# Optimization experiments

Measured on AMD Instinct MI355X. Metric: run time of the kernel, lower is better.

The kernel has to match this reference:

```python
import jax, jax.numpy as jnp
import numpy as np

D_MODEL, D_K, D_V = 1024, 64, 64
B, S = 4, 4096

def setup_inputs() -> dict:
    key = jax.random.key(0)
    ks = jax.random.split(key, 9)
    s_in = 1.0 / np.sqrt(D_MODEL)
    return {
        "Q": jax.random.normal(ks[0], (B, S, D_MODEL), jnp.float32),
        "K": jax.random.normal(ks[1], (B, S, D_MODEL), jnp.float32),
        "V": jax.random.normal(ks[2], (B, S, D_MODEL), jnp.float32),
        "Wq": jax.random.uniform(ks[3], (D_MODEL, D_K), jnp.float32, -s_in, s_in),
        "bq": jax.random.uniform(ks[4], (D_K,), jnp.float32, -s_in, s_in),
        "Wk": jax.random.uniform(ks[5], (D_MODEL, D_K), jnp.float32, -s_in, s_in),
        "bk": jax.random.uniform(ks[6], (D_K,), jnp.float32, -s_in, s_in),
        "Wv": jax.random.uniform(ks[7], (D_MODEL, D_V), jnp.float32, -s_in, s_in),
        "bv": jax.random.uniform(ks[8], (D_V,), jnp.float32, -s_in, s_in),
    }

def reference(Q, K, V, Wq, bq, Wk, bk, Wv, bv):
    # Linear projections: [B,S,d_model] -> [B,S,d_k/d_v]
    q = jnp.einsum("bsm,mk->bsk", Q, Wq) + bq
    k = jnp.einsum("btm,mk->btk", K, Wk) + bk
    v = jnp.einsum("btm,mv->btv", V, Wv) + bv
    # Scaled dot-product attention, softmax over key axis (dim=2)
    scores = jnp.einsum("bsk,btk->bst", q, k) / jnp.sqrt(jnp.float32(D_K))
    attn = jax.nn.softmax(scores, axis=2)  # [B,S,S]
    return jnp.einsum("bst,btv->bsv", attn, v)
```

## Files before the change

### kernel.cpp

```cpp
#include <hip/hip_runtime.h>

typedef __bf16 bf16;
typedef __attribute__((ext_vector_type(8))) __bf16 bf16x8;
typedef __attribute__((ext_vector_type(4))) float f32x4;
typedef __attribute__((ext_vector_type(16))) float f32x16;

#define MFMA16(a, b, c) __builtin_amdgcn_mfma_f32_16x16x32_bf16((a), (b), (c), 0, 0, 0)
#define MFMA32(a, b, c) __builtin_amdgcn_mfma_f32_32x32x16_bf16((a), (b), (c), 0, 0, 0)

__device__ __forceinline__ bf16 tobf(float f) {
    unsigned u = __float_as_uint(f);
    u += 0x7fffu + ((u >> 16) & 1u);
    unsigned short h = (unsigned short)(u >> 16);
    bf16 r;
    __builtin_memcpy(&r, &h, 2);
    return r;
}

__device__ __forceinline__ bf16x8 cvt8h(f32x4 a, f32x4 b) {
    bf16x8 r;
    r[0] = (bf16)a[0]; r[1] = (bf16)a[1]; r[2] = (bf16)a[2]; r[3] = (bf16)a[3];
    r[4] = (bf16)b[0]; r[5] = (bf16)b[1]; r[6] = (bf16)b[2]; r[7] = (bf16)b[3];
    return r;
}

__global__ void wconv_kernel(const float* __restrict__ Wq, const float* __restrict__ Wk,
                             const float* __restrict__ Wv, bf16* __restrict__ Wt) {
    int j = blockIdx.y;
    const float* W = (j == 0) ? Wq : ((j == 1) ? Wk : Wv);
    int idx = blockIdx.x * 256 + threadIdx.x;
    int m = idx >> 6, n = idx & 63;
    Wt[(size_t)j * 65536 + (size_t)n * 1024 + m] = tobf(W[idx]);
}

__launch_bounds__(256, 4)
__global__ void proj_kernel(const float* __restrict__ Q, const float* __restrict__ K,
                            const float* __restrict__ V, const bf16* __restrict__ Wt,
                            const float* __restrict__ bq, const float* __restrict__ bk,
                            const float* __restrict__ bv,
                            bf16* __restrict__ q_ws, bf16* __restrict__ k_ws,
                            bf16* __restrict__ vT_ws) {
    const int j = blockIdx.y;
    const float* In   = (j == 0) ? Q : ((j == 1) ? K : V);
    const float* bias = (j == 0) ? bq : ((j == 1) ? bk : bv);
    const bf16* W = Wt + (size_t)j * 65536;

    __shared__ bf16 vtile[64][72];

    const int tid = threadIdx.x;
    const int wave = tid >> 6, lane = tid & 63;
    const int quad = lane >> 4, l16 = lane & 15;
    const int rbase = blockIdx.x * 64 + wave * 16;

    const float* arow = In + (size_t)(rbase + l16) * 1024 + quad * 8;
    const bf16* wbase = W + quad * 8;

    f32x4 acc[4];
#pragma unroll
    for (int nt = 0; nt < 4; nt++) acc[nt] = {0.f, 0.f, 0.f, 0.f};

    f32x4 a0 = *(const f32x4*)(arow);
    f32x4 a1 = *(const f32x4*)(arow + 4);
    f32x4 a2 = *(const f32x4*)(arow + 32);
    f32x4 a3 = *(const f32x4*)(arow + 36);

    for (int kc = 0; kc < 1024; kc += 64) {
        bf16x8 av0 = cvt8h(a0, a1);
        bf16x8 av1 = cvt8h(a2, a3);
        if (kc + 64 < 1024) {
            a0 = *(const f32x4*)(arow + kc + 64);
            a1 = *(const f32x4*)(arow + kc + 68);
            a2 = *(const f32x4*)(arow + kc + 96);
            a3 = *(const f32x4*)(arow + kc + 100);
        }
#pragma unroll
        for (int nt = 0; nt < 4; nt++) {
            const bf16* wp = wbase + (size_t)(nt * 16 + l16) * 1024 + kc;
            bf16x8 b0 = *(const bf16x8*)(wp);
            bf16x8 b1 = *(const bf16x8*)(wp + 32);
            acc[nt] = MFMA16(av0, b0, acc[nt]);
            acc[nt] = MFMA16(av1, b1, acc[nt]);
        }
    }

    const float scale = (j == 0) ? 0.125f * 1.44269504088896f : 1.0f;

    if (j != 2) {
        bf16* dst = (j == 0) ? q_ws : k_ws;
#pragma unroll
        for (int nt = 0; nt < 4; nt++) {
            int n = nt * 16 + l16;
            float bb = bias[n];
#pragma unroll
            for (int r = 0; r < 4; r++) {
                int row = rbase + quad * 4 + r;
                dst[(size_t)row * 64 + n] = tobf((acc[nt][r] + bb) * scale);
            }
        }
    } else {
#pragma unroll
        for (int nt = 0; nt < 4; nt++) {
            int n = nt * 16 + l16;
            float bb = bias[n];
#pragma unroll
            for (int r = 0; r < 4; r++) {
                vtile[n][wave * 16 + quad * 4 + r] = tobf(acc[nt][r] + bb);
            }
        }
        __syncthreads();
        int gb = blockIdx.x * 64;
        int bi = gb >> 12, t0 = gb & 4095;
        int d = tid >> 2, part = (tid & 3) * 16;
        bf16x8 x0 = *(const bf16x8*)&vtile[d][part];
        bf16x8 x1 = *(const bf16x8*)&vtile[d][part + 8];
        bf16* dst = vT_ws + (size_t)(bi * 64 + d) * 4096 + t0 + part;
        *(bf16x8*)dst = x0;
        *(bf16x8*)(dst + 8) = x1;
    }
}

__launch_bounds__(256, 3)
__global__ void attn_kernel(const bf16* __restrict__ q_ws, const bf16* __restrict__ k_ws,
                            const bf16* __restrict__ vT_ws,
                            float* __restrict__ po, float* __restrict__ pl,
                            float* __restrict__ out, int keys_per_split, int direct) {
    const int b = blockIdx.z, split = blockIdx.y;
    const int tid = threadIdx.x, wave = tid >> 6, lane = tid & 63;
    const int l32 = lane & 31, h = lane >> 5;

    __shared__ bf16 kt[64][80];
    __shared__ bf16 vt[64][80];
    __shared__ bf16 pt[4][32][72];

    const int qrow0 = b * 4096 + blockIdx.x * 128 + wave * 32;

    bf16x8 qf[4];
    const bf16* qp = q_ws + (size_t)(qrow0 + l32) * 64 + h * 8;
#pragma unroll
    for (int c = 0; c < 4; c++) qf[c] = *(const bf16x8*)(qp + c * 16);

    f32x16 o0, o1;
    float l[16];
#pragma unroll
    for (int i = 0; i < 16; i++) { o0[i] = 0.f; o1[i] = 0.f; l[i] = 0.f; }

    const int key0 = split * keys_per_split;
    const int srow = tid >> 3, scol = (tid & 7) * 8;
    const bf16* kg = k_ws + (size_t)(b * 4096 + key0 + srow) * 64 + scol;
    const bf16* vg = vT_ws + (size_t)(b * 64 + srow) * 4096 + key0 + scol;

    uint4 kv0 = *(const uint4*)kg;
    uint4 kv1 = *(const uint4*)(kg + 2048);
    uint4 vv0 = *(const uint4*)vg;
    uint4 vv1 = *(const uint4*)(vg + 131072);

    for (int t0 = 0; t0 < keys_per_split; t0 += 64) {
        __syncthreads();
        *(uint4*)&kt[srow][scol]      = kv0;
        *(uint4*)&kt[srow + 32][scol] = kv1;
        *(uint4*)&vt[srow][scol]      = vv0;
        *(uint4*)&vt[srow + 32][scol] = vv1;
        if (t0 + 64 < keys_per_split) {
            kv0 = *(const uint4*)(kg + (size_t)(t0 + 64) * 64);
            kv1 = *(const uint4*)(kg + (size_t)(t0 + 64) * 64 + 2048);
            vv0 = *(const uint4*)(vg + t0 + 64);
            vv1 = *(const uint4*)(vg + t0 + 64 + 131072);
        }
        __syncthreads();

#pragma unroll
        for (int kt32 = 0; kt32 < 2; kt32++) {
            f32x16 s;
#pragma unroll
            for (int i = 0; i < 16; i++) s[i] = 0.f;
#pragma unroll
            for (int c = 0; c < 4; c++) {
                bf16x8 kf = *(const bf16x8*)(&kt[kt32 * 32 + l32][c * 16 + h * 8]);
                s = MFMA32(qf[c], kf, s);
            }
#pragma unroll
            for (int i = 0; i < 16; i++) {
                float p = __builtin_amdgcn_exp2f(s[i]);
                l[i] += p;
                int R = (i & 3) + 8 * (i >> 2) + 4 * h;
                pt[wave][R][kt32 * 32 + l32] = (bf16)p;
            }
        }

#pragma unroll
        for (int tc = 0; tc < 4; tc++) {
            bf16x8 pf  = *(const bf16x8*)(&pt[wave][l32][tc * 16 + h * 8]);
            bf16x8 vf0 = *(const bf16x8*)(&vt[l32][tc * 16 + h * 8]);
            bf16x8 vf1 = *(const bf16x8*)(&vt[32 + l32][tc * 16 + h * 8]);
            o0 = MFMA32(pf, vf0, o0);
            o1 = MFMA32(pf, vf1, o1);
        }
    }

#pragma unroll
    for (int i = 0; i < 16; i++) {
        float v = l[i];
        v += __shfl_xor(v, 1);  v += __shfl_xor(v, 2);  v += __shfl_xor(v, 4);
        v += __shfl_xor(v, 8);  v += __shfl_xor(v, 16);
        l[i] = v;
    }

    if (direct) {
        float* orow = out + (size_t)qrow0 * 64;
#pragma unroll
        for (int i = 0; i < 16; i++) {
            int R = (i & 3) + 8 * (i >> 2) + 4 * h;
            float inv = 1.0f / l[i];
            orow[(size_t)R * 64 + l32]      = o0[i] * inv;
            orow[(size_t)R * 64 + 32 + l32] = o1[i] * inv;
        }
    } else {
        size_t prow = (size_t)split * 16384 + qrow0;
        float* pob = po + prow * 64;
#pragma unroll
        for (int i = 0; i < 16; i++) {
            int R = (i & 3) + 8 * (i >> 2) + 4 * h;
            pob[(size_t)R * 64 + l32]      = o0[i];
            pob[(size_t)R * 64 + 32 + l32] = o1[i];
            if (l32 == 0) pl[prow + R] = l[i];
        }
    }
}

__launch_bounds__(256)
__global__ void combine_kernel(const float* __restrict__ po, const float* __restrict__ pl,
                               float* __restrict__ out, int nsplit) {
    int idx = blockIdx.x * 256 + threadIdx.x;
    int row = idx >> 6;
    float so = 0.f, sl = 0.f;
    for (int s = 0; s < nsplit; s++) {
        so += po[(size_t)s * 1048576 + idx];
        sl += pl[(size_t)s * 16384 + row];
    }
    out[idx] = so / sl;
}

extern "C" void kernel_launch(void* const* d_in, const int* in_sizes, int n_in,
                              void* d_out, int out_size, void* d_ws, size_t ws_size,
                              hipStream_t stream) {
    const float* Q  = (const float*)d_in[0];
    const float* K  = (const float*)d_in[1];
    const float* V  = (const float*)d_in[2];
    const float* Wq = (const float*)d_in[3];
    const float* bq = (const float*)d_in[4];
    const float* Wk = (const float*)d_in[5];
    const float* bk = (const float*)d_in[6];
    const float* Wv = (const float*)d_in[7];
    const float* bv = (const float*)d_in[8];
    float* out = (float*)d_out;

    char* ws = (char*)d_ws;
    bf16* Wt    = (bf16*)ws;
    bf16* q_ws  = (bf16*)(ws + 393216);
    bf16* k_ws  = (bf16*)(ws + 393216 + 2097152);
    bf16* vT_ws = (bf16*)(ws + 393216 + 2 * 2097152);
    const size_t base = 393216 + 3 * 2097152;

    const size_t per_split = 16384u * 4u + 1048576u * 4u;
    int nsplit = 1;
    if (ws_size >= base + 8 * per_split) nsplit = 8;
    else if (ws_size >= base + 4 * per_split) nsplit = 4;
    else if (ws_size >= base + 2 * per_split) nsplit = 2;

    float* pl = (float*)(ws + base);
    float* po = (float*)(ws + base + (size_t)nsplit * 65536);

    hipLaunchKernelGGL(wconv_kernel, dim3(256, 3), dim3(256), 0, stream, Wq, Wk, Wv, Wt);
    hipLaunchKernelGGL(proj_kernel, dim3(256, 3), dim3(256), 0, stream,
                       Q, K, V, Wt, bq, bk, bv, q_ws, k_ws, vT_ws);
    hipLaunchKernelGGL(attn_kernel, dim3(32, nsplit, 4), dim3(256), 0, stream,
                       q_ws, k_ws, vT_ws, po, pl, out, 4096 / nsplit, nsplit == 1 ? 1 : 0);
    if (nsplit > 1) {
        hipLaunchKernelGGL(combine_kernel, dim3(4096), dim3(256), 0, stream, po, pl, out, nsplit);
    }
}
```

Baseline: 273.7 us.

## Stage projection tiles through LDS with direct global-to-LDS loads and XOR swizzle

The projection kernel now copies 64x128 fp32 input tiles and 64x128 bf16 weight tiles into shared memory using global_load_lds with an XOR swizzle, then feeds the MFMAs from LDS. Before, each lane read global memory directly with a register prefetch. The aim is coalesced bulk loads and weight reuse across the four waves, at the cost of two barriers per k-chunk and no overlap between loading and compute. Launch bounds are also swapped (proj to 3 blocks per CU, attn to 4), and attn's K/V LDS row padding shrinks from 80 to 72.

```diff
diff --git a/kernel.cpp b/kernel.cpp
--- a/kernel.cpp
+++ b/kernel.cpp
@@ -7,6 +7,13 @@
 
 #define MFMA16(a, b, c) __builtin_amdgcn_mfma_f32_16x16x32_bf16((a), (b), (c), 0, 0, 0)
 #define MFMA32(a, b, c) __builtin_amdgcn_mfma_f32_32x32x16_bf16((a), (b), (c), 0, 0, 0)
+
+typedef __attribute__((address_space(3))) unsigned int lds_u32_t;
+typedef __attribute__((address_space(1))) unsigned int glb_u32_t;
+
+__device__ __forceinline__ void gl2lds16(const void* g, void* l) {
+    __builtin_amdgcn_global_load_lds((const glb_u32_t*)g, (lds_u32_t*)l, 16, 0, 0);
+}
 
 __device__ __forceinline__ bf16 tobf(float f) {
     unsigned u = __float_as_uint(f);
@@ -33,7 +40,7 @@
     Wt[(size_t)j * 65536 + (size_t)n * 1024 + m] = tobf(W[idx]);
 }
 
-__launch_bounds__(256, 4)
+__launch_bounds__(256, 3)
 __global__ void proj_kernel(const float* __restrict__ Q, const float* __restrict__ K,
                             const float* __restrict__ V, const bf16* __restrict__ Wt,
                             const float* __restrict__ bq, const float* __restrict__ bk,
@@ -45,42 +52,55 @@
     const float* bias = (j == 0) ? bq : ((j == 1) ? bk : bv);
     const bf16* W = Wt + (size_t)j * 65536;
 
-    __shared__ bf16 vtile[64][72];
+    __shared__ char smem[49152];
+    char* As = smem;
+    char* Bs = smem + 32768;
 
     const int tid = threadIdx.x;
     const int wave = tid >> 6, lane = tid & 63;
     const int quad = lane >> 4, l16 = lane & 15;
-    const int rbase = blockIdx.x * 64 + wave * 16;
-
-    const float* arow = In + (size_t)(rbase + l16) * 1024 + quad * 8;
-    const bf16* wbase = W + quad * 8;
+    const int rbase_blk = blockIdx.x * 64;
 
     f32x4 acc[4];
 #pragma unroll
     for (int nt = 0; nt < 4; nt++) acc[nt] = {0.f, 0.f, 0.f, 0.f};
 
-    f32x4 a0 = *(const f32x4*)(arow);
-    f32x4 a1 = *(const f32x4*)(arow + 4);
-    f32x4 a2 = *(const f32x4*)(arow + 32);
-    f32x4 a3 = *(const f32x4*)(arow + 36);
-
-    for (int kc = 0; kc < 1024; kc += 64) {
-        bf16x8 av0 = cvt8h(a0, a1);
-        bf16x8 av1 = cvt8h(a2, a3);
-        if (kc + 64 < 1024) {
-            a0 = *(const f32x4*)(arow + kc + 64);
-            a1 = *(const f32x4*)(arow + kc + 68);
-            a2 = *(const f32x4*)(arow + kc + 96);
-            a3 = *(const f32x4*)(arow + kc + 100);
-        }
-#pragma unroll
-        for (int nt = 0; nt < 4; nt++) {
-            const bf16* wp = wbase + (size_t)(nt * 16 + l16) * 1024 + kc;
-            bf16x8 b0 = *(const bf16x8*)(wp);
-            bf16x8 b1 = *(const bf16x8*)(wp + 32);
-            acc[nt] = MFMA16(av0, b0, acc[nt]);
-            acc[nt] = MFMA16(av1, b1, acc[nt]);
-        }
+    for (int kc = 0; kc < 1024; kc += 128) {
+#pragma unroll
+        for (int i = 0; i < 8; i++) {
+            int u = i * 256 + tid;
+            int row = u >> 5, cg = u & 31;
+            int cgg = cg ^ (row & 31);
+            const float* g = In + (size_t)(rbase_blk + row) * 1024 + kc + cgg * 4;
+            gl2lds16(g, As + (size_t)(i * 256 + wave * 64) * 16);
+        }
+#pragma unroll
+        for (int i = 0; i < 4; i++) {
+            int u = i * 256 + tid;
+            int n = u >> 4, cg = u & 15;
+            int cgg = cg ^ (n & 15);
+            const bf16* g = W + (size_t)n * 1024 + kc + cgg * 8;
+            gl2lds16(g, Bs + (size_t)(i * 256 + wave * 64) * 16);
+        }
+        __syncthreads();
+
+        const int r = wave * 16 + l16;
+#pragma unroll
+        for (int p = 0; p < 4; p++) {
+            int cg0 = (p * 8 + quad * 2) ^ (r & 31);
+            int cg1 = (p * 8 + quad * 2 + 1) ^ (r & 31);
+            f32x4 a0 = *(const f32x4*)(As + (size_t)r * 512 + cg0 * 16);
+            f32x4 a1 = *(const f32x4*)(As + (size_t)r * 512 + cg1 * 16);
+            bf16x8 av = cvt8h(a0, a1);
+#pragma unroll
+            for (int nt = 0; nt < 4; nt++) {
+                int n = nt * 16 + l16;
+                int cgb = (p * 4 + quad) ^ (n & 15);
+                bf16x8 bv = *(const bf16x8*)(Bs + (size_t)n * 256 + cgb * 16);
+                acc[nt] = MFMA16(av, bv, acc[nt]);
+            }
+        }
+        __syncthreads();
     }
 
     const float scale = (j == 0) ? 0.125f * 1.44269504088896f : 1.0f;
@@ -92,23 +112,24 @@
             int n = nt * 16 + l16;
             float bb = bias[n];
 #pragma unroll
-            for (int r = 0; r < 4; r++) {
-                int row = rbase + quad * 4 + r;
-                dst[(size_t)row * 64 + n] = tobf((acc[nt][r] + bb) * scale);
+            for (int r4 = 0; r4 < 4; r4++) {
+                int row = rbase_blk + wave * 16 + quad * 4 + r4;
+                dst[(size_t)row * 64 + n] = tobf((acc[nt][r4] + bb) * scale);
             }
         }
     } else {
+        bf16 (*vtile)[72] = (bf16(*)[72])smem;
 #pragma unroll
         for (int nt = 0; nt < 4; nt++) {
             int n = nt * 16 + l16;
             float bb = bias[n];
 #pragma unroll
-            for (int r = 0; r < 4; r++) {
-                vtile[n][wave * 16 + quad * 4 + r] = tobf(acc[nt][r] + bb);
-            }
-        }
-        __syncthreads();
-        int gb = blockIdx.x * 64;
+            for (int r4 = 0; r4 < 4; r4++) {
+                vtile[n][wave * 16 + quad * 4 + r4] = tobf(acc[nt][r4] + bb);
+            }
+        }
+        __syncthreads();
+        int gb = rbase_blk;
         int bi = gb >> 12, t0 = gb & 4095;
         int d = tid >> 2, part = (tid & 3) * 16;
         bf16x8 x0 = *(const bf16x8*)&vtile[d][part];
@@ -119,7 +140,7 @@
     }
 }
 
-__launch_bounds__(256, 3)
+__launch_bounds__(256, 4)
 __global__ void attn_kernel(const bf16* __restrict__ q_ws, const bf16* __restrict__ k_ws,
                             const bf16* __restrict__ vT_ws,
                             float* __restrict__ po, float* __restrict__ pl,
@@ -128,8 +149,8 @@
     const int tid = threadIdx.x, wave = tid >> 6, lane = tid & 63;
     const int l32 = lane & 31, h = lane >> 5;
 
-    __shared__ bf16 kt[64][80];
-    __shared__ bf16 vt[64][80];
+    __shared__ bf16 kt[64][72];
+    __shared__ bf16 vt[64][72];
     __shared__ bf16 pt[4][32][72];
 
     const int qrow0 = b * 4096 + blockIdx.x * 128 + wave * 32;
```

Result: faster. 260.3 us (-4.9%).
